# Kernel optimization log

Hardware: AMD Instinct MI355X
Metric: run time of the kernel (lower is better)

Reference implementation:

```python
import jax, jax.numpy as jnp
import numpy as np

MARGIN = 0.5


def setup_inputs() -> dict:
    key = jax.random.key(0)
    k1, k2, k3 = jax.random.split(key, 3)
    B, D = 8192, 128
    anchor = jax.random.normal(k1, (B, D), dtype=jnp.float32)
    positive = jax.random.normal(k2, (B, D), dtype=jnp.float32)
    labels = jax.random.randint(k3, (B,), 0, 100, dtype=jnp.int64)
    return {"anchor": anchor, "positive": positive, "labels": labels}


def _l2_normalize(x, eps=1e-12):
    # matches F.normalize(p=2, dim=1): x / max(||x||, eps)
    n = jnp.sqrt(jnp.sum(x * x, axis=1, keepdims=True))
    return x / jnp.maximum(n, eps)


def reference(anchor, positive, labels):
    a = _l2_normalize(anchor)   # [B, D]
    p = _l2_normalize(positive)  # [B, D]

    # pairwise euclidean distances among normalized anchors:
    # ||a_i - a_j||^2 = 2 - 2 a_i . a_j  (unit vectors)
    gram = jnp.einsum('id,jd->ij', a, a)              # [B, B]
    dist = jnp.sqrt(jnp.maximum(2.0 - 2.0 * gram, 0.0))

    # mask out same-label pairs (includes diagonal)
    same = labels[None, :] == labels[:, None]
    dist = jnp.where(same, jnp.inf, dist)

    min_dist = jnp.min(dist, axis=1)                  # [B]
    neg_dist = min_dist * min_dist                    # squared distance to hard negative

    pos_dist = jnp.sum((a - p) ** 2, axis=1)          # [B]

    loss = jax.nn.relu(pos_dist - neg_dist + MARGIN)
    return jnp.mean(loss)
```

## Files before the change

### kernel.cpp

```cpp
#include <hip/hip_runtime.h>
#include <stdint.h>

#define NROWS 8192
#define DIM 128

typedef __bf16 bf16x8 __attribute__((ext_vector_type(8)));
typedef float floatx4 __attribute__((ext_vector_type(4)));

static __device__ __forceinline__ unsigned short f2bf(float f) {
    unsigned int u = __float_as_uint(f);
    unsigned int r = (u + 0x7FFFu + ((u >> 16) & 1u)) >> 16;
    return (unsigned short)r;
}

static __device__ __forceinline__ int swz(int g) {
    return (g & ~15) | ((g & 15) ^ ((g >> 4) & 7));
}

__global__ __launch_bounds__(256) void normalize_kernel(
    const float* __restrict__ anchor, const float* __restrict__ positive,
    unsigned short* __restrict__ a_hat, float* __restrict__ pos_ws,
    int* __restrict__ g_ws)
{
    const int wave = threadIdx.x >> 6;
    const int lane = threadIdx.x & 63;
    const int row  = blockIdx.x * 4 + wave;

    const float2* arow = (const float2*)(anchor   + row * DIM);
    const float2* prow = (const float2*)(positive + row * DIM);
    float2 a = arow[lane];
    float2 p = prow[lane];

    float sa  = a.x * a.x + a.y * a.y;
    float sp  = p.x * p.x + p.y * p.y;
    float sap = a.x * p.x + a.y * p.y;
    #pragma unroll
    for (int off = 32; off; off >>= 1) {
        sa  += __shfl_xor(sa,  off);
        sp  += __shfl_xor(sp,  off);
        sap += __shfl_xor(sap, off);
    }
    float na  = fmaxf(sqrtf(sa), 1e-12f);
    float npn = fmaxf(sqrtf(sp), 1e-12f);
    float inv = 1.0f / na;

    ushort2 pack;
    pack.x = f2bf(a.x * inv);
    pack.y = f2bf(a.y * inv);
    ((ushort2*)a_hat)[row * 64 + lane] = pack;

    if (lane == 0) {
        pos_ws[row] = 2.0f - 2.0f * sap / (na * npn);
        g_ws[row]   = 0x3F800000;
    }
}

__global__ __launch_bounds__(256, 4) void gram_kernel(
    const unsigned short* __restrict__ a_hat, const int* __restrict__ labels,
    int* __restrict__ g_ws)
{
    const int tid  = threadIdx.x;
    const int lane = tid & 63;
    const int wave = tid >> 6;
    const int quad = lane >> 4;
    const int l15  = lane & 15;

    const int rowBlock = blockIdx.x >> 4;
    const int nchunk   = blockIdx.x & 15;
    const int rowBase  = rowBlock * 128 + wave * 32;

    const uint4* A = (const uint4*)a_hat;

    __shared__ uint4 smem[2][512];

    bf16x8 afrag[2][4];
    #pragma unroll
    for (int s = 0; s < 2; ++s) {
        int r = rowBase + s * 16 + l15;
        #pragma unroll
        for (int k = 0; k < 4; ++k) {
            uint4 v = A[r * 16 + k * 4 + quad];
            afrag[s][k] = __builtin_bit_cast(bf16x8, v);
        }
    }

    int rlab[2][4];
    #pragma unroll
    for (int s = 0; s < 2; ++s)
        #pragma unroll
        for (int e = 0; e < 4; ++e)
            rlab[s][e] = labels[rowBase + s * 16 + quad * 4 + e];

    float gmax[2][4];
    #pragma unroll
    for (int s = 0; s < 2; ++s)
        #pragma unroll
        for (int e = 0; e < 4; ++e)
            gmax[s][e] = -4.0f;

    const int colBase = nchunk * 512;
    const uint4* Gp = A + colBase * 16;

    uint4 p0 = Gp[tid];
    uint4 p1 = Gp[tid + 256];
    smem[0][swz(tid)]       = p0;
    smem[0][swz(tid + 256)] = p1;
    __syncthreads();

    for (int cb = 0; cb < 16; ++cb) {
        const int cur = cb & 1;

        if (cb < 15) {
            p0 = Gp[(cb + 1) * 512 + tid];
            p1 = Gp[(cb + 1) * 512 + tid + 256];
        }

        const int C = colBase + cb * 32;
        int clab0 = labels[C + l15];
        int clab1 = labels[C + 16 + l15];

        bf16x8 bfrag[2][4];
        #pragma unroll
        for (int ns = 0; ns < 2; ++ns) {
            int c = ns * 16 + l15;
            #pragma unroll
            for (int k = 0; k < 4; ++k) {
                int g = c * 16 + k * 4 + quad;
                bfrag[ns][k] = __builtin_bit_cast(bf16x8, smem[cur][swz(g)]);
            }
        }

        #pragma unroll
        for (int ms = 0; ms < 2; ++ms) {
            #pragma unroll
            for (int ns = 0; ns < 2; ++ns) {
                floatx4 acc = {0.f, 0.f, 0.f, 0.f};
                #pragma unroll
                for (int k = 0; k < 4; ++k)
                    acc = __builtin_amdgcn_mfma_f32_16x16x32_bf16(
                              afrag[ms][k], bfrag[ns][k], acc, 0, 0, 0);
                const int cl = ns ? clab1 : clab0;
                #pragma unroll
                for (int e = 0; e < 4; ++e) {
                    float v = (cl != rlab[ms][e]) ? acc[e] : -4.0f;
                    gmax[ms][e] = fmaxf(gmax[ms][e], v);
                }
            }
        }

        if (cb < 15) {
            smem[cur ^ 1][swz(tid)]       = p0;
            smem[cur ^ 1][swz(tid + 256)] = p1;
            __syncthreads();
        }
    }

    #pragma unroll
    for (int s = 0; s < 2; ++s) {
        #pragma unroll
        for (int e = 0; e < 4; ++e) {
            float v = gmax[s][e];
            #pragma unroll
            for (int off = 1; off < 16; off <<= 1)
                v = fmaxf(v, __shfl_xor(v, off));
            if (l15 == 0) {
                int r = rowBase + s * 16 + quad * 4 + e;
                atomicMax(g_ws + r, __float_as_int(2.0f + v));
            }
        }
    }
}

__global__ __launch_bounds__(256) void loss_kernel(
    const float* __restrict__ pos_ws, const int* __restrict__ g_ws,
    float* __restrict__ out)
{
    const int i = blockIdx.x * 256 + threadIdx.x;
    float g    = __int_as_float(g_ws[i]) - 2.0f;
    float neg  = fmaxf(2.0f - 2.0f * g, 0.0f);
    float loss = fmaxf(pos_ws[i] - neg + 0.5f, 0.0f);

    #pragma unroll
    for (int off = 32; off; off >>= 1)
        loss += __shfl_xor(loss, off);

    __shared__ float ws[4];
    if ((threadIdx.x & 63) == 0) ws[threadIdx.x >> 6] = loss;
    __syncthreads();
    if (threadIdx.x == 0) {
        float s = ws[0] + ws[1] + ws[2] + ws[3];
        atomicAdd(out, s * (1.0f / 8192.0f));
    }
}

extern "C" void kernel_launch(void* const* d_in, const int* in_sizes, int n_in,
                              void* d_out, int out_size, void* d_ws, size_t ws_size,
                              hipStream_t stream) {
    const float* anchor   = (const float*)d_in[0];
    const float* positive = (const float*)d_in[1];
    const int*   labels   = (const int*)d_in[2];
    float* out = (float*)d_out;

    char* ws = (char*)d_ws;
    unsigned short* a_hat  = (unsigned short*)ws;
    float*          pos_ws = (float*)(ws + 2 * 1024 * 1024);
    int*            g_ws   = (int*)  (ws + 2 * 1024 * 1024 + 32 * 1024);

    hipMemsetAsync(d_out, 0, sizeof(float), stream);
    normalize_kernel<<<NROWS / 4, 256, 0, stream>>>(anchor, positive, a_hat, pos_ws, g_ws);
    gram_kernel<<<1024, 256, 0, stream>>>(a_hat, labels, g_ws);
    loss_kernel<<<NROWS / 256, 256, 0, stream>>>(pos_ws, g_ws, out);
}
```

Measured before the change: 88.26 us.

## Enlarge gram tile to 64 rows per wave and 64-column stages

Each wave now covers 64 anchor rows instead of 32, and every pipeline stage loads 64 columns into a doubled shared buffer, halving the grid to 512 blocks. This raises MFMA work per LDS fragment load and per barrier, and halves the redundant column reads across row blocks. The cost is more registers (launch bounds lowered to 2 blocks per SM), lower occupancy, and fewer blocks to spread over 256 CUs, which may leave some CUs idle.

```diff
diff --git a/kernel.cpp b/kernel.cpp
--- a/kernel.cpp
+++ b/kernel.cpp
@@ -55,7 +55,7 @@
     }
 }
 
-__global__ __launch_bounds__(256, 4) void gram_kernel(
+__global__ __launch_bounds__(256, 2) void gram_kernel(
     const unsigned short* __restrict__ a_hat, const int* __restrict__ labels,
     int* __restrict__ g_ws)
 {
@@ -67,15 +67,15 @@
 
     const int rowBlock = blockIdx.x >> 4;
     const int nchunk   = blockIdx.x & 15;
-    const int rowBase  = rowBlock * 128 + wave * 32;
+    const int rowBase  = rowBlock * 256 + wave * 64;
 
     const uint4* A = (const uint4*)a_hat;
 
-    __shared__ uint4 smem[2][512];
-
-    bf16x8 afrag[2][4];
-    #pragma unroll
-    for (int s = 0; s < 2; ++s) {
+    __shared__ uint4 smem[2][1024];
+
+    bf16x8 afrag[4][4];
+    #pragma unroll
+    for (int s = 0; s < 4; ++s) {
         int r = rowBase + s * 16 + l15;
         #pragma unroll
         for (int k = 0; k < 4; ++k) {
@@ -84,16 +84,16 @@
         }
     }
 
-    int rlab[2][4];
-    #pragma unroll
-    for (int s = 0; s < 2; ++s)
+    int rlab[4][4];
+    #pragma unroll
+    for (int s = 0; s < 4; ++s)
         #pragma unroll
         for (int e = 0; e < 4; ++e)
             rlab[s][e] = labels[rowBase + s * 16 + quad * 4 + e];
 
-    float gmax[2][4];
-    #pragma unroll
-    for (int s = 0; s < 2; ++s)
+    float gmax[4][4];
+    #pragma unroll
+    for (int s = 0; s < 4; ++s)
         #pragma unroll
         for (int e = 0; e < 4; ++e)
             gmax[s][e] = -4.0f;
@@ -103,60 +103,75 @@
 
     uint4 p0 = Gp[tid];
     uint4 p1 = Gp[tid + 256];
+    uint4 p2 = Gp[tid + 512];
+    uint4 p3 = Gp[tid + 768];
     smem[0][swz(tid)]       = p0;
     smem[0][swz(tid + 256)] = p1;
+    smem[0][swz(tid + 512)] = p2;
+    smem[0][swz(tid + 768)] = p3;
     __syncthreads();
 
-    for (int cb = 0; cb < 16; ++cb) {
-        const int cur = cb & 1;
-
-        if (cb < 15) {
-            p0 = Gp[(cb + 1) * 512 + tid];
-            p1 = Gp[(cb + 1) * 512 + tid + 256];
-        }
-
-        const int C = colBase + cb * 32;
-        int clab0 = labels[C + l15];
-        int clab1 = labels[C + 16 + l15];
-
-        bf16x8 bfrag[2][4];
-        #pragma unroll
-        for (int ns = 0; ns < 2; ++ns) {
-            int c = ns * 16 + l15;
-            #pragma unroll
-            for (int k = 0; k < 4; ++k) {
-                int g = c * 16 + k * 4 + quad;
-                bfrag[ns][k] = __builtin_bit_cast(bf16x8, smem[cur][swz(g)]);
-            }
-        }
-
-        #pragma unroll
-        for (int ms = 0; ms < 2; ++ms) {
+    for (int st = 0; st < 8; ++st) {
+        const int cur = st & 1;
+
+        if (st < 7) {
+            const uint4* Gn = Gp + (st + 1) * 1024;
+            p0 = Gn[tid];
+            p1 = Gn[tid + 256];
+            p2 = Gn[tid + 512];
+            p3 = Gn[tid + 768];
+        }
+
+        const int C = colBase + st * 64;
+        int clab[4];
+        #pragma unroll
+        for (int t = 0; t < 4; ++t)
+            clab[t] = labels[C + t * 16 + l15];
+
+        #pragma unroll
+        for (int sub = 0; sub < 2; ++sub) {
+            bf16x8 bfrag[2][4];
             #pragma unroll
             for (int ns = 0; ns < 2; ++ns) {
-                floatx4 acc = {0.f, 0.f, 0.f, 0.f};
+                int c = sub * 32 + ns * 16 + l15;
                 #pragma unroll
-                for (int k = 0; k < 4; ++k)
-                    acc = __builtin_amdgcn_mfma_f32_16x16x32_bf16(
-                              afrag[ms][k], bfrag[ns][k], acc, 0, 0, 0);
-                const int cl = ns ? clab1 : clab0;
-                #pragma unroll
-                for (int e = 0; e < 4; ++e) {
-                    float v = (cl != rlab[ms][e]) ? acc[e] : -4.0f;
-                    gmax[ms][e] = fmaxf(gmax[ms][e], v);
+                for (int k = 0; k < 4; ++k) {
+                    int g = c * 16 + k * 4 + quad;
+                    bfrag[ns][k] = __builtin_bit_cast(bf16x8, smem[cur][swz(g)]);
                 }
             }
-        }
-
-        if (cb < 15) {
-            smem[cur ^ 1][swz(tid)]       = p0;
-            smem[cur ^ 1][swz(tid + 256)] = p1;
+
+            #pragma unroll
+            for (int ms = 0; ms < 4; ++ms) {
+                #pragma unroll
+                for (int ns = 0; ns < 2; ++ns) {
+                    floatx4 acc = {0.f, 0.f, 0.f, 0.f};
+                    #pragma unroll
+                    for (int k = 0; k < 4; ++k)
+                        acc = __builtin_amdgcn_mfma_f32_16x16x32_bf16(
+                                  afrag[ms][k], bfrag[ns][k], acc, 0, 0, 0);
+                    const int cl = clab[sub * 2 + ns];
+                    #pragma unroll
+                    for (int e = 0; e < 4; ++e) {
+                        float v = (cl != rlab[ms][e]) ? acc[e] : -4.0f;
+                        gmax[ms][e] = fmaxf(gmax[ms][e], v);
+                    }
+                }
+            }
+        }
+
+        if (st < 7) {
+            const int nxt = cur ^ 1;
+            smem[nxt][swz(tid)]       = p0;
+            smem[nxt][swz(tid + 256)] = p1;
+            smem[nxt][swz(tid + 512)] = p2;
+            smem[nxt][swz(tid + 768)] = p3;
             __syncthreads();
         }
     }
 
     #pragma unroll
-    for (int s = 0; s < 2; ++s) {
+    for (int s = 0; s < 4; ++s) {
         #pragma unroll
         for (int e = 0; e < 4; ++e) {
             float v = gmax[s][e];
@@ -208,6 +223,6 @@
 
     hipMemsetAsync(d_out, 0, sizeof(float), stream);
     normalize_kernel<<<NROWS / 4, 256, 0, stream>>>(anchor, positive, a_hat, pos_ws, g_ws);
-    gram_kernel<<<1024, 256, 0, stream>>>(a_hat, labels, g_ws);
+    gram_kernel<<<512, 256, 0, stream>>>(a_hat, labels, g_ws);
     loss_kernel<<<NROWS / 256, 256, 0, stream>>>(pos_ws, g_ws, out);
 }
```

Measured after the change: 89.04 us. Within noise of the previous version (+0.9%).
